# Optimization experiments

Hardware: AMD Instinct MI355X
Metric: run time of the kernel (lower is better)

## Reference

```python
import jax, jax.numpy as jnp
import numpy as np

B = 8192
D_IN = 512
D_HID = 256
D_OUT = 128
EPS_STD = 1e-5
EPS_NORM = 1e-12


def _embed(x, W1, b1, W2, b2):
    # head: Linear -> ReLU -> Linear
    h = jax.nn.relu(x @ W1 + b1)          # (b, 256)
    y = h @ W2 + b2                        # (b, 128)
    # white(): per-feature batch whitening (center + unit std, unbiased like torch.std)
    mu = jnp.mean(y, axis=0, keepdims=True)
    sd = jnp.std(y, axis=0, keepdims=True, ddof=1) + EPS_STD
    y = (y - mu) / sd
    # F.normalize(p=2, dim=1)
    n = jnp.maximum(jnp.linalg.norm(y, axis=1, keepdims=True), EPS_NORM)
    return y / n


def _pair_loss(v1, v2):
    b = v1.shape[0]
    cat = jnp.concatenate([v1, v2], axis=0)            # (2b, d)
    inner = v1 @ cat.T                                  # (b, 2b) == broadcasted (v1*cat).sum(2)
    mask = jnp.concatenate(
        [1.0 - jnp.eye(b, dtype=inner.dtype), jnp.ones((b, b), dtype=inner.dtype)], axis=1)
    logits = inner * mask                               # zero out self-similarity logits
    logp = jax.nn.log_softmax(logits, axis=1)
    tgt = jnp.arange(b, 2 * b)                          # positive = matching row in v2 block
    return -jnp.take_along_axis(logp, tgt[:, None], axis=1).mean()


def setup_inputs() -> dict:
    key = jax.random.key(0)
    ks = jax.random.split(key, 16)
    def lin_init(k, fin, fout):
        bound = 1.0 / np.sqrt(fin)
        kw, kb = jax.random.split(k)
        W = jax.random.uniform(kw, (fin, fout), jnp.float32, -bound, bound)
        b = jax.random.uniform(kb, (fout,), jnp.float32, -bound, bound)
        return W, b
    inp = {
        'x_B': jax.random.normal(ks[0], (B, D_IN), jnp.float32),
        'x_E': jax.random.normal(ks[1], (B, D_IN), jnp.float32),
        'x_F': jax.random.normal(ks[2], (B, D_IN), jnp.float32),
    }
    for i, m in enumerate('BEF'):
        W1, b1 = lin_init(ks[3 + 2 * i], D_IN, D_HID)
        W2, b2 = lin_init(ks[4 + 2 * i], D_HID, D_OUT)
        inp[f'W1_{m}'] = W1; inp[f'b1_{m}'] = b1
        inp[f'W2_{m}'] = W2; inp[f'b2_{m}'] = b2
    return inp


def reference(x_B, x_E, x_F,
              W1_B, b1_B, W2_B, b2_B,
              W1_E, b1_E, W2_E, b2_E,
              W1_F, b1_F, W2_F, b2_F):
    zB = _embed(x_B, W1_B, b1_B, W2_B, b2_B)
    zE = _embed(x_E, W1_E, b1_E, W2_E, b2_E)
    zF = _embed(x_F, W1_F, b1_F, W2_F, b2_F)
    pairs = [(zB, zE), (zB, zF), (zE, zF)]  # itertools.combinations order
    loss = sum(_pair_loss(v1, v2) for v1, v2 in pairs) / len(pairs)
    return loss
```

## Files before the change

kernel.cpp:

```cpp
#include <hip/hip_runtime.h>
#include <hip/hip_bf16.h>
#include <math.h>

#define NROWS 8192
#define DIN   512
#define DHID  256
#define DOUT  128
#define LOG2E 1.4426950408889634f

typedef unsigned short ushort_t;
typedef __attribute__((ext_vector_type(8))) short bf16x8;
typedef __attribute__((ext_vector_type(4))) float f32x4;

#if defined(__has_builtin)
#  if __has_builtin(__builtin_amdgcn_exp2f)
#    define FAST_EXP2(x) __builtin_amdgcn_exp2f(x)
#  else
#    define FAST_EXP2(x) exp2f(x)
#  endif
#else
#  define FAST_EXP2(x) exp2f(x)
#endif

__device__ __forceinline__ short f2bf(float x) {
  __hip_bfloat16 h = __float2bfloat16(x);
  return *(short*)&h;
}

__device__ __forceinline__ float bf2f(ushort_t v) {
  unsigned int u = ((unsigned int)v) << 16;
  union { unsigned int u; float f; } c; c.u = u;
  return c.f;
}

__device__ __forceinline__ bf16x8 cvt8(float4 lo, float4 hi) {
  bf16x8 r;
  r[0] = f2bf(lo.x); r[1] = f2bf(lo.y); r[2] = f2bf(lo.z); r[3] = f2bf(lo.w);
  r[4] = f2bf(hi.x); r[5] = f2bf(hi.y); r[6] = f2bf(hi.z); r[7] = f2bf(hi.w);
  return r;
}

__device__ __forceinline__ void dma16(const void* g, void* l) {
  __builtin_amdgcn_global_load_lds(
      (const __attribute__((address_space(1))) unsigned int*)g,
      (__attribute__((address_space(3))) unsigned int*)l, 16, 0, 0);
}

__global__ __launch_bounds__(256) void prep_w_kernel(
    const float* __restrict__ W1_0, const float* __restrict__ W1_1,
    const float* __restrict__ W1_2,
    const float* __restrict__ W2_0, const float* __restrict__ W2_1,
    const float* __restrict__ W2_2,
    ushort_t* __restrict__ w1t3, ushort_t* __restrict__ w2t3,
    float* __restrict__ zero_region, float* __restrict__ out)
{
  const int z = blockIdx.z, gx = blockIdx.x, gy = blockIdx.y;
  const int tid = threadIdx.x;
  if (z == 0) {
    int b = gy * 4 + gx;
#pragma unroll
    for (int j = 0; j < 4; j++) {
      int idx = b * 256 + tid + j * 12288;
      if (idx < 41728) zero_region[idx] = 0.0f;
    }
    if (b == 0 && tid == 0) out[0] = 0.0f;
  }
  const float* W1 = z == 0 ? W1_0 : (z == 1 ? W1_1 : W1_2);
  const float* W2 = z == 0 ? W2_0 : (z == 1 ? W2_1 : W2_2);

  __shared__ float t[64][65];
  if (gy < 8) {
    const int k0 = gy * 64, n0 = gx * 64;
#pragma unroll
    for (int it = 0; it < 16; it++) {
      int r = it * 4 + (tid >> 6), c = tid & 63;
      t[r][c] = W1[(size_t)(k0 + r) * DHID + n0 + c];
    }
    __syncthreads();
    ushort_t* dst = w1t3 + (size_t)z * DHID * DIN;
#pragma unroll
    for (int it = 0; it < 16; it++) {
      int n = it * 4 + (tid >> 6), k = tid & 63;
      dst[(size_t)(n0 + n) * DIN + k0 + k] = (ushort_t)f2bf(t[k][n]);
    }
  } else {
    if (gx >= 2) return;
    const int k0 = (gy - 8) * 64, n0 = gx * 64;
#pragma unroll
    for (int it = 0; it < 16; it++) {
      int r = it * 4 + (tid >> 6), c = tid & 63;
      t[r][c] = W2[(size_t)(k0 + r) * DOUT + n0 + c];
    }
    __syncthreads();
    ushort_t* dst = w2t3 + (size_t)z * DOUT * DHID;
#pragma unroll
    for (int it = 0; it < 16; it++) {
      int n = it * 4 + (tid >> 6), k = tid & 63;
      dst[(size_t)(n0 + n) * DHID + k0 + k] = (ushort_t)f2bf(t[k][n]);
    }
  }
}

#define MLP_BUF 24576
__global__ __launch_bounds__(256, 2) void mlp_kernel(
    const float* __restrict__ x0, const float* __restrict__ x1,
    const float* __restrict__ x2,
    const ushort_t* __restrict__ w1t3,
    const float* __restrict__ b1_0, const float* __restrict__ b1_1,
    const float* __restrict__ b1_2,
    const ushort_t* __restrict__ w2t3,
    const float* __restrict__ b2_0, const float* __restrict__ b2_1,
    const float* __restrict__ b2_2,
    ushort_t* __restrict__ y3,
    float* __restrict__ colsum, float* __restrict__ colsumsq)
{
  const int z = blockIdx.y;
  const float* X  = z == 0 ? x0 : (z == 1 ? x1 : x2);
  const float* B1 = z == 0 ? b1_0 : (z == 1 ? b1_1 : b1_2);
  const float* B2 = z == 0 ? b2_0 : (z == 1 ? b2_1 : b2_2);
  const ushort_t* W1t = w1t3 + (size_t)z * DHID * DIN;
  const ushort_t* W2t = w2t3 + (size_t)z * DOUT * DHID;
  ushort_t* Y = y3 + (size_t)z * NROWS * DOUT;
  float* csum = colsum + z * DOUT;
  float* csq  = colsumsq + z * DOUT;

  __shared__ __align__(16) char lds[2 * MLP_BUF];
  ushort_t* hs = (ushort_t*)lds;

  const int tid = threadIdx.x, lane = tid & 63, wave = tid >> 6;
  const int quad = lane >> 4, l16 = lane & 15;
  const int m0 = blockIdx.x * 64;

  const char* w1b = (const char*)W1t;
  const char* wsrc[4];
#pragma unroll
  for (int jj = 0; jj < 4; jj++)
    wsrc[jj] = w1b + (size_t)(16 * (wave * 4 + jj) + l16) * 1024 + quad * 16;
  const int row8 = lane >> 3, slot = lane & 7;
  const int gseg = (slot + row8) & 7;
  const char* xsrc[2];
#pragma unroll
  for (int jj = 0; jj < 2; jj++)
    xsrc[jj] = (const char*)X +
        (size_t)(m0 + 8 * (wave * 2 + jj) + row8) * 2048 + gseg * 16;

  f32x4 acc1[4][4] = {};
#pragma unroll
  for (int jj = 0; jj < 4; jj++)
    dma16(wsrc[jj], lds + (wave * 4 + jj) * 1024);
#pragma unroll
  for (int jj = 0; jj < 2; jj++)
    dma16(xsrc[jj], lds + 16384 + (wave * 2 + jj) * 1024);
  __syncthreads();

  for (int c = 0; c < 16; c++) {
    const int buf = c & 1;
    if (c + 1 < 16) {
      char* dst = lds + (buf ^ 1) * MLP_BUF;
#pragma unroll
      for (int jj = 0; jj < 4; jj++)
        dma16(wsrc[jj] + (c + 1) * 64, dst + (wave * 4 + jj) * 1024);
#pragma unroll
      for (int jj = 0; jj < 2; jj++)
        dma16(xsrc[jj] + (c + 1) * 128, dst + 16384 + (wave * 2 + jj) * 1024);
    }
    const char* wb = lds + buf * MLP_BUF;
    const char* xb = wb + 16384;
    bf16x8 a[4];
#pragma unroll
    for (int mt = 0; mt < 4; mt++) {
      const int r = mt * 16 + l16, r7 = r & 7;
      const int s0 = (2 * quad - r7) & 7, s1 = (2 * quad + 1 - r7) & 7;
      float4 v0 = *(const float4*)(xb + r * 128 + s0 * 16);
      float4 v1 = *(const float4*)(xb + r * 128 + s1 * 16);
      a[mt] = cvt8(v0, v1);
    }
    bf16x8 b[4];
#pragma unroll
    for (int ct = 0; ct < 4; ct++)
      b[ct] = *(const bf16x8*)(wb + (wave * 4 + ct) * 1024 + quad * 256 +
                               l16 * 16);
#pragma unroll
    for (int mt = 0; mt < 4; mt++)
#pragma unroll
      for (int ct = 0; ct < 4; ct++)
        acc1[mt][ct] = __builtin_amdgcn_mfma_f32_16x16x32_bf16(
            a[mt], b[ct], acc1[mt][ct], 0, 0, 0);
    __syncthreads();
  }

  bf16x8 b2f[2][8];
#pragma unroll
  for (int ct = 0; ct < 2; ct++)
#pragma unroll
    for (int kk = 0; kk < 8; kk++)
      b2f[ct][kk] = *(const bf16x8*)(W2t +
          (size_t)(wave * 32 + ct * 16 + l16) * DHID + kk * 32 + quad * 8);

#pragma unroll
  for (int ct = 0; ct < 4; ct++) {
    float bb = B1[wave * 64 + ct * 16 + l16];
#pragma unroll
    for (int mt = 0; mt < 4; mt++)
#pragma unroll
      for (int reg = 0; reg < 4; reg++) {
        float v = fmaxf(acc1[mt][ct][reg] + bb, 0.0f);
        hs[(mt * 16 + quad * 4 + reg) * 264 + wave * 64 + ct * 16 + l16] =
            (ushort_t)f2bf(v);
      }
  }
  __syncthreads();

  f32x4 acc2[4][2] = {};
#pragma unroll
  for (int kk = 0; kk < 8; kk++) {
    bf16x8 a2[4];
#pragma unroll
    for (int mt = 0; mt < 4; mt++)
      a2[mt] = *(const bf16x8*)(hs + (mt * 16 + l16) * 264 + kk * 32 +
                                quad * 8);
#pragma unroll
    for (int mt = 0; mt < 4; mt++)
#pragma unroll
      for (int ct = 0; ct < 2; ct++)
        acc2[mt][ct] = __builtin_amdgcn_mfma_f32_16x16x32_bf16(
            a2[mt], b2f[ct][kk], acc2[mt][ct], 0, 0, 0);
  }

#pragma unroll
  for (int ct = 0; ct < 2; ct++) {
    const int colo = wave * 32 + ct * 16 + l16;
    float bb = B2[colo];
    float cs = 0.0f, cq = 0.0f;
#pragma unroll
    for (int mt = 0; mt < 4; mt++)
#pragma unroll
      for (int reg = 0; reg < 4; reg++) {
        float v = acc2[mt][ct][reg] + bb;
        Y[(size_t)(m0 + mt * 16 + quad * 4 + reg) * DOUT + colo] =
            (ushort_t)f2bf(v);
        cs += v; cq += v * v;
      }
    cs += __shfl_xor(cs, 16, 64); cs += __shfl_xor(cs, 32, 64);
    cq += __shfl_xor(cq, 16, 64); cq += __shfl_xor(cq, 32, 64);
    if (lane < 16) {
      atomicAdd(&csum[colo], cs);
      atomicAdd(&csq[colo], cq);
    }
  }
}

__global__ __launch_bounds__(256) void whiten_kernel(
    const ushort_t* __restrict__ y3,
    const float* __restrict__ colsum, const float* __restrict__ colsumsq,
    ushort_t* __restrict__ zB, ushort_t* __restrict__ zE,
    ushort_t* __restrict__ zF,
    ushort_t* __restrict__ zBs, ushort_t* __restrict__ zEs,
    float* __restrict__ pos)
{
  const int tid = threadIdx.x, lane = tid & 63, wave = tid >> 6;
  const int row = blockIdx.x * 4 + wave;
  const size_t base = (size_t)row * DOUT;
  const size_t hsz = (size_t)NROWS * DOUT;
  const int c0 = lane, c1 = lane + 64;

  float mu[3][2], isd[3][2];
#pragma unroll
  for (int h = 0; h < 3; h++) {
#pragma unroll
    for (int cc = 0; cc < 2; cc++) {
      const int idx = h * DOUT + (cc ? c1 : c0);
      float m = colsum[idx] * (1.0f / NROWS);
      float var = (colsumsq[idx] - (float)NROWS * m * m) *
                  (1.0f / (NROWS - 1));
      mu[h][cc] = m;
      isd[h][cc] = 1.0f / (sqrtf(fmaxf(var, 0.0f)) + 1e-5f);
    }
  }

  float vB0 = (bf2f(y3[base + c0])           - mu[0][0]) * isd[0][0];
  float vB1 = (bf2f(y3[base + c1])           - mu[0][1]) * isd[0][1];
  float vE0 = (bf2f(y3[base + hsz + c0])     - mu[1][0]) * isd[1][0];
  float vE1 = (bf2f(y3[base + hsz + c1])     - mu[1][1]) * isd[1][1];
  float vF0 = (bf2f(y3[base + 2 * hsz + c0]) - mu[2][0]) * isd[2][0];
  float vF1 = (bf2f(y3[base + 2 * hsz + c1]) - mu[2][1]) * isd[2][1];

  float nB = vB0 * vB0 + vB1 * vB1;
  float nE = vE0 * vE0 + vE1 * vE1;
  float nF = vF0 * vF0 + vF1 * vF1;
#pragma unroll
  for (int o = 1; o < 64; o <<= 1) {
    nB += __shfl_xor(nB, o, 64);
    nE += __shfl_xor(nE, o, 64);
    nF += __shfl_xor(nF, o, 64);
  }
  float iB = 1.0f / fmaxf(sqrtf(nB), 1e-12f);
  float iE = 1.0f / fmaxf(sqrtf(nE), 1e-12f);
  float iF = 1.0f / fmaxf(sqrtf(nF), 1e-12f);
  float zb0 = vB0 * iB, zb1 = vB1 * iB;
  float ze0 = vE0 * iE, ze1 = vE1 * iE;
  float zf0 = vF0 * iF, zf1 = vF1 * iF;

  zB[base + c0]  = (ushort_t)f2bf(zb0);
  zB[base + c1]  = (ushort_t)f2bf(zb1);
  zE[base + c0]  = (ushort_t)f2bf(ze0);
  zE[base + c1]  = (ushort_t)f2bf(ze1);
  zF[base + c0]  = (ushort_t)f2bf(zf0);
  zF[base + c1]  = (ushort_t)f2bf(zf1);
  zBs[base + c0] = (ushort_t)f2bf(zb0 * LOG2E);
  zBs[base + c1] = (ushort_t)f2bf(zb1 * LOG2E);
  zEs[base + c0] = (ushort_t)f2bf(ze0 * LOG2E);
  zEs[base + c1] = (ushort_t)f2bf(ze1 * LOG2E);

  float pBE = zb0 * ze0 + zb1 * ze1;
  float pBF = zb0 * zf0 + zb1 * zf1;
  float pEF = ze0 * zf0 + ze1 * zf1;
#pragma unroll
  for (int o = 1; o < 64; o <<= 1) {
    pBE += __shfl_xor(pBE, o, 64);
    pBF += __shfl_xor(pBF, o, 64);
    pEF += __shfl_xor(pEF, o, 64);
  }
  if (lane == 0) {
    pos[row]             = pBE;
    pos[NROWS + row]     = pBF;
    pos[2 * NROWS + row] = pEF;
  }
}

#define G_CH  32
#define G_NCH 32
__global__ __launch_bounds__(256, 3) void gram_kernel(
    const ushort_t* __restrict__ zB, const ushort_t* __restrict__ zE,
    const ushort_t* __restrict__ zF,
    const ushort_t* __restrict__ zBs, const ushort_t* __restrict__ zEs,
    float* __restrict__ rowsum)
{
  const ushort_t *U, *V;
  float* rs;
  switch (blockIdx.z) {
    case 0:  U = zBs; V = zB; rs = rowsum;             break;
    case 1:  U = zEs; V = zE; rs = rowsum + NROWS;     break;
    case 2:  U = zBs; V = zE; rs = rowsum + 2 * NROWS; break;
    case 3:  U = zBs; V = zF; rs = rowsum + 3 * NROWS; break;
    default: U = zEs; V = zF; rs = rowsum + 4 * NROWS; break;
  }

  const int tid = threadIdx.x, lane = tid & 63, wave = tid >> 6;
  const int quad = lane >> 4, l16 = lane & 15;
  const int m0 = blockIdx.x * 256 + wave * 64;
  const int col0 = blockIdx.y * (G_CH * G_NCH);

  __shared__ __align__(16) ushort_t sbuf[2][4096];

  const ushort_t* ua = U + (size_t)(m0 + l16) * DOUT + quad * 8;
  bf16x8 a[4][4];
#pragma unroll
  for (int rt = 0; rt < 4; rt++)
#pragma unroll
    for (int ki = 0; ki < 4; ki++)
      a[rt][ki] = *(const bf16x8*)(ua + rt * 16 * DOUT + ki * 32);

  const char* Vb = (const char*)V;
  const int r_ = lane & 31, hi_ = lane >> 5;
  const int s0 = 4 * wave + hi_, s1 = 4 * wave + 2 + hi_;
  const char* g0 = Vb + (size_t)(col0 + r_) * 256 + (s0 >> 2) * 64 + (s0 & 3) * 16;
  const char* g1 = Vb + (size_t)(col0 + r_) * 256 + (s1 >> 2) * 64 + (s1 & 3) * 16;

  float rsum[4][4] = {};
  const f32x4 zero = {0.0f, 0.0f, 0.0f, 0.0f};

  dma16(g0, &sbuf[0][(2 * wave) * 512]);
  dma16(g1, &sbuf[0][(2 * wave + 1) * 512]);
  __syncthreads();

  for (int c = 0; c < G_NCH; c++) {
    const int buf = c & 1;
    if (c + 1 < G_NCH) {
      const size_t go = (size_t)(c + 1) * 8192;
      dma16(g0 + go, &sbuf[buf ^ 1][(2 * wave) * 512]);
      dma16(g1 + go, &sbuf[buf ^ 1][(2 * wave + 1) * 512]);
    }
    const char* sb = (const char*)&sbuf[buf][0];
    bf16x8 b[4][2];
#pragma unroll
    for (int ki = 0; ki < 4; ki++)
#pragma unroll
      for (int ct = 0; ct < 2; ct++)
        b[ki][ct] = *(const bf16x8*)(sb + (ki * 4 + quad) * 512 +
                                     (ct * 16 + l16) * 16);
    f32x4 acc[4][2];
#pragma unroll
    for (int ki = 0; ki < 4; ki++)
#pragma unroll
      for (int rt = 0; rt < 4; rt++)
#pragma unroll
        for (int ct = 0; ct < 2; ct++)
          acc[rt][ct] = __builtin_amdgcn_mfma_f32_16x16x32_bf16(
              a[rt][ki], b[ki][ct], ki == 0 ? zero : acc[rt][ct], 0, 0, 0);
#pragma unroll
    for (int rt = 0; rt < 4; rt++)
#pragma unroll
      for (int reg = 0; reg < 4; reg++)
        rsum[rt][reg] += FAST_EXP2(acc[rt][0][reg]) + FAST_EXP2(acc[rt][1][reg]);
    __syncthreads();
  }

#pragma unroll
  for (int rt = 0; rt < 4; rt++)
#pragma unroll
    for (int reg = 0; reg < 4; reg++) {
      float s = rsum[rt][reg];
      s += __shfl_xor(s, 1, 64);
      s += __shfl_xor(s, 2, 64);
      s += __shfl_xor(s, 4, 64);
      s += __shfl_xor(s, 8, 64);
      if (l16 == 0)
        atomicAdd(&rs[m0 + rt * 16 + quad * 4 + reg], s);
    }
}

__global__ __launch_bounds__(256) void loss_kernel(
    const float* __restrict__ rowsum, const float* __restrict__ pos,
    float* __restrict__ out)
{
  const float* sB  = rowsum;
  const float* sE  = rowsum + NROWS;
  const float* cBE = rowsum + 2 * NROWS;
  const float* cBF = rowsum + 3 * NROWS;
  const float* cEF = rowsum + 4 * NROWS;
  const float* pBE = pos;
  const float* pBF = pos + NROWS;
  const float* pEF = pos + 2 * NROWS;

  const int i = blockIdx.x * 256 + threadIdx.x;
  const float corr = 1.0f - expf(1.0f);
  float selB = sB[i] + corr;
  float selE = sE[i] + corr;
  float local = __logf(selB + cBE[i]) - pBE[i];
  local += __logf(selB + cBF[i]) - pBF[i];
  local += __logf(selE + cEF[i]) - pEF[i];

  __shared__ float red[4];
#pragma unroll
  for (int o = 32; o > 0; o >>= 1) local += __shfl_down(local, o, 64);
  int lane = threadIdx.x & 63, wv = threadIdx.x >> 6;
  if (lane == 0) red[wv] = local;
  __syncthreads();
  if (threadIdx.x == 0) {
    float t = red[0] + red[1] + red[2] + red[3];
    atomicAdd(out, t * (1.0f / (3.0f * (float)NROWS)));
  }
}

extern "C" void kernel_launch(void* const* d_in, const int* in_sizes, int n_in,
                              void* d_out, int out_size, void* d_ws, size_t ws_size,
                              hipStream_t stream)
{
  const float* xs[3] = {(const float*)d_in[0], (const float*)d_in[1], (const float*)d_in[2]};
  const float* W1[3] = {(const float*)d_in[3], (const float*)d_in[7],  (const float*)d_in[11]};
  const float* b1[3] = {(const float*)d_in[4], (const float*)d_in[8],  (const float*)d_in[12]};
  const float* W2[3] = {(const float*)d_in[5], (const float*)d_in[9],  (const float*)d_in[13]};
  const float* b2[3] = {(const float*)d_in[6], (const float*)d_in[10], (const float*)d_in[14]};

  float* ws = (float*)d_ws;
  float* colsum   = ws;
  float* colsumsq = ws + 384;
  float* rowsum   = ws + 768;
  float* pos      = ws + 42496;
  ushort_t* w1t3 = (ushort_t*)(ws + 67072);
  ushort_t* w2t3 = (ushort_t*)(ws + 263680);
  ushort_t* y3b  = (ushort_t*)(ws + 312832);
  ushort_t* zB   = (ushort_t*)(ws + 1885696);
  ushort_t* zE   = zB  + (size_t)NROWS * DOUT;
  ushort_t* zF   = zE  + (size_t)NROWS * DOUT;
  ushort_t* zBs  = zF  + (size_t)NROWS * DOUT;
  ushort_t* zEs  = zBs + (size_t)NROWS * DOUT;

  prep_w_kernel<<<dim3(4, 12, 3), 256, 0, stream>>>(
      W1[0], W1[1], W1[2], W2[0], W2[1], W2[2], w1t3, w2t3, ws, (float*)d_out);
  mlp_kernel<<<dim3(128, 3), 256, 0, stream>>>(
      xs[0], xs[1], xs[2], w1t3, b1[0], b1[1], b1[2],
      w2t3, b2[0], b2[1], b2[2], y3b, colsum, colsumsq);
  whiten_kernel<<<2048, 256, 0, stream>>>(
      y3b, colsum, colsumsq, zB, zE, zF, zBs, zEs, pos);
  gram_kernel<<<dim3(32, 8, 5), 256, 0, stream>>>(zB, zE, zF, zBs, zEs, rowsum);
  loss_kernel<<<32, 256, 0, stream>>>(rowsum, pos, (float*)d_out);
}
```

Before: 219.3 us.

## Exploit Gram symmetry for self-similarity blocks and fuse loss into gram kernel

Self-similarity Gram products (B·B, E·E) now compute only upper-triangle 256x256 tiles, adding exp column sums of off-diagonal tiles via atomics to the mirrored rows, which roughly halves that work. Work is remapped to a flat 1D grid mixing full cross-pair blocks and triangular self blocks. The separate loss kernel is removed: the last gram block, detected via an atomic counter, computes the final log-sum reduction. This adds extra atomics and shuffles per chunk and relies on near-symmetry of the scaled bf16 inputs.

Measured after the change: 265.2 us. 20.9% more time.

```diff
diff --git a/kernel.cpp b/kernel.cpp
--- a/kernel.cpp
+++ b/kernel.cpp
@@ -61,7 +61,7 @@
 #pragma unroll
     for (int j = 0; j < 4; j++) {
       int idx = b * 256 + tid + j * 12288;
-      if (idx < 41728) zero_region[idx] = 0.0f;
+      if (idx < 41792) zero_region[idx] = 0.0f;
     }
     if (b == 0 && tid == 0) out[0] = 0.0f;
   }
@@ -328,17 +328,33 @@
   }
 }
 
-#define G_CH  32
-#define G_NCH 32
+#define NBLK_GRAM 1824
 __global__ __launch_bounds__(256, 3) void gram_kernel(
     const ushort_t* __restrict__ zB, const ushort_t* __restrict__ zE,
     const ushort_t* __restrict__ zF,
     const ushort_t* __restrict__ zBs, const ushort_t* __restrict__ zEs,
-    float* __restrict__ rowsum)
+    float* __restrict__ rowsum, const float* __restrict__ pos,
+    unsigned int* __restrict__ counter, float* __restrict__ out)
 {
+  const int id = blockIdx.x;
+  int combo, mblk, cbase, nch, do_col;
+  if (id < 768) {
+    combo = 2 + (id >> 8);
+    const int r = id & 255;
+    mblk = r >> 3; cbase = (r & 7) * 1024; nch = 32; do_col = 0;
+  } else {
+    const int sid = id - 768;
+    combo = sid / 528;
+    int t = sid - combo * 528;
+    int p = 0, acc0 = 0;
+    while (acc0 + (32 - p) <= t) { acc0 += 32 - p; p++; }
+    const int q = p + (t - acc0);
+    mblk = p; cbase = q << 8; nch = 8; do_col = (q > p);
+  }
+
   const ushort_t *U, *V;
   float* rs;
-  switch (blockIdx.z) {
+  switch (combo) {
     case 0:  U = zBs; V = zB; rs = rowsum;             break;
     case 1:  U = zEs; V = zE; rs = rowsum + NROWS;     break;
     case 2:  U = zBs; V = zE; rs = rowsum + 2 * NROWS; break;
@@ -348,8 +364,7 @@
 
   const int tid = threadIdx.x, lane = tid & 63, wave = tid >> 6;
   const int quad = lane >> 4, l16 = lane & 15;
-  const int m0 = blockIdx.x * 256 + wave * 64;
-  const int col0 = blockIdx.y * (G_CH * G_NCH);
+  const int m0 = mblk * 256 + wave * 64;
 
   __shared__ __align__(16) ushort_t sbuf[2][4096];
 
@@ -364,8 +379,8 @@
   const char* Vb = (const char*)V;
   const int r_ = lane & 31, hi_ = lane >> 5;
   const int s0 = 4 * wave + hi_, s1 = 4 * wave + 2 + hi_;
-  const char* g0 = Vb + (size_t)(col0 + r_) * 256 + (s0 >> 2) * 64 + (s0 & 3) * 16;
-  const char* g1 = Vb + (size_t)(col0 + r_) * 256 + (s1 >> 2) * 64 + (s1 & 3) * 16;
+  const char* g0 = Vb + (size_t)(cbase + r_) * 256 + s0 * 16;
+  const char* g1 = Vb + (size_t)(cbase + r_) * 256 + s1 * 16;
 
   float rsum[4][4] = {};
   const f32x4 zero = {0.0f, 0.0f, 0.0f, 0.0f};
@@ -374,9 +389,9 @@
   dma16(g1, &sbuf[0][(2 * wave + 1) * 512]);
   __syncthreads();
 
-  for (int c = 0; c < G_NCH; c++) {
+  for (int c = 0; c < nch; c++) {
     const int buf = c & 1;
-    if (c + 1 < G_NCH) {
+    if (c + 1 < nch) {
       const size_t go = (size_t)(c + 1) * 8192;
       dma16(g0 + go, &sbuf[buf ^ 1][(2 * wave) * 512]);
       dma16(g1 + go, &sbuf[buf ^ 1][(2 * wave + 1) * 512]);
@@ -398,11 +413,25 @@
         for (int ct = 0; ct < 2; ct++)
           acc[rt][ct] = __builtin_amdgcn_mfma_f32_16x16x32_bf16(
               a[rt][ki], b[ki][ct], ki == 0 ? zero : acc[rt][ct], 0, 0, 0);
+    float csum0 = 0.0f, csum1 = 0.0f;
 #pragma unroll
     for (int rt = 0; rt < 4; rt++)
 #pragma unroll
-      for (int reg = 0; reg < 4; reg++)
-        rsum[rt][reg] += FAST_EXP2(acc[rt][0][reg]) + FAST_EXP2(acc[rt][1][reg]);
+      for (int reg = 0; reg < 4; reg++) {
+        float e0 = FAST_EXP2(acc[rt][0][reg]);
+        float e1 = FAST_EXP2(acc[rt][1][reg]);
+        rsum[rt][reg] += e0 + e1;
+        csum0 += e0; csum1 += e1;
+      }
+    if (do_col) {
+      csum0 += __shfl_xor(csum0, 16, 64); csum0 += __shfl_xor(csum0, 32, 64);
+      csum1 += __shfl_xor(csum1, 16, 64); csum1 += __shfl_xor(csum1, 32, 64);
+      if (quad == 0) {
+        const int colc = cbase + c * 32;
+        atomicAdd(&rs[colc + l16], csum0);
+        atomicAdd(&rs[colc + 16 + l16], csum1);
+      }
+    }
     __syncthreads();
   }
 
@@ -418,38 +447,42 @@
       if (l16 == 0)
         atomicAdd(&rs[m0 + rt * 16 + quad * 4 + reg], s);
     }
-}
-
-__global__ __launch_bounds__(256) void loss_kernel(
-    const float* __restrict__ rowsum, const float* __restrict__ pos,
-    float* __restrict__ out)
-{
-  const float* sB  = rowsum;
-  const float* sE  = rowsum + NROWS;
-  const float* cBE = rowsum + 2 * NROWS;
-  const float* cBF = rowsum + 3 * NROWS;
-  const float* cEF = rowsum + 4 * NROWS;
-  const float* pBE = pos;
-  const float* pBF = pos + NROWS;
-  const float* pEF = pos + 2 * NROWS;
-
-  const int i = blockIdx.x * 256 + threadIdx.x;
-  const float corr = 1.0f - expf(1.0f);
-  float selB = sB[i] + corr;
-  float selE = sE[i] + corr;
-  float local = __logf(selB + cBE[i]) - pBE[i];
-  local += __logf(selB + cBF[i]) - pBF[i];
-  local += __logf(selE + cEF[i]) - pEF[i];
-
-  __shared__ float red[4];
-#pragma unroll
-  for (int o = 32; o > 0; o >>= 1) local += __shfl_down(local, o, 64);
-  int lane = threadIdx.x & 63, wv = threadIdx.x >> 6;
-  if (lane == 0) red[wv] = local;
+
+  __shared__ int is_last;
   __syncthreads();
-  if (threadIdx.x == 0) {
-    float t = red[0] + red[1] + red[2] + red[3];
-    atomicAdd(out, t * (1.0f / (3.0f * (float)NROWS)));
+  if (tid == 0) {
+    __threadfence();
+    unsigned int old = atomicAdd(counter, 1u);
+    is_last = (old == (unsigned int)(NBLK_GRAM - 1)) ? 1 : 0;
+  }
+  __syncthreads();
+  if (is_last) {
+    __threadfence();
+    const float corr = 1.0f - expf(1.0f);
+    float local = 0.0f;
+    for (int i = tid; i < NROWS; i += 256) {
+      float sB = __hip_atomic_load(&rowsum[i], __ATOMIC_RELAXED,
+                                   __HIP_MEMORY_SCOPE_AGENT) + corr;
+      float sE = __hip_atomic_load(&rowsum[NROWS + i], __ATOMIC_RELAXED,
+                                   __HIP_MEMORY_SCOPE_AGENT) + corr;
+      float cBE = __hip_atomic_load(&rowsum[2 * NROWS + i], __ATOMIC_RELAXED,
+                                    __HIP_MEMORY_SCOPE_AGENT);
+      float cBF = __hip_atomic_load(&rowsum[3 * NROWS + i], __ATOMIC_RELAXED,
+                                    __HIP_MEMORY_SCOPE_AGENT);
+      float cEF = __hip_atomic_load(&rowsum[4 * NROWS + i], __ATOMIC_RELAXED,
+                                    __HIP_MEMORY_SCOPE_AGENT);
+      local += __logf(sB + cBE) - pos[i];
+      local += __logf(sB + cBF) - pos[NROWS + i];
+      local += __logf(sE + cEF) - pos[2 * NROWS + i];
+    }
+    __shared__ float red[4];
+#pragma unroll
+    for (int o = 32; o > 0; o >>= 1) local += __shfl_down(local, o, 64);
+    if (lane == 0) red[wave] = local;
+    __syncthreads();
+    if (tid == 0)
+      out[0] = (red[0] + red[1] + red[2] + red[3]) *
+               (1.0f / (3.0f * (float)NROWS));
   }
 }
 
@@ -467,6 +500,7 @@
   float* colsum   = ws;
   float* colsumsq = ws + 384;
   float* rowsum   = ws + 768;
+  unsigned int* counter = (unsigned int*)(ws + 41728);
   float* pos      = ws + 42496;
   ushort_t* w1t3 = (ushort_t*)(ws + 67072);
   ushort_t* w2t3 = (ushort_t*)(ws + 263680);
@@ -484,6 +518,6 @@
       w2t3, b2[0], b2[1], b2[2], y3b, colsum, colsumsq);
   whiten_kernel<<<2048, 256, 0, stream>>>(
       y3b, colsum, colsumsq, zB, zE, zF, zBs, zEs, pos);
-  gram_kernel<<<dim3(32, 8, 5), 256, 0, stream>>>(zB, zE, zF, zBs, zEs, rowsum);
-  loss_kernel<<<32, 256, 0, stream>>>(rowsum, pos, (float*)d_out);
-}
+  gram_kernel<<<NBLK_GRAM, 256, 0, stream>>>(
+      zB, zE, zF, zBs, zEs, rowsum, pos, counter, (float*)d_out);
+}
```
